# Performance work log

Measured on AMD Instinct MI355X. Metric: run time of the kernel, lower is better.

## Reference

```python
import jax, jax.numpy as jnp
import numpy as np

N = 50000      # nodes
E = 1600000    # edges
L = 128        # latent_size


def _mlp(h, W1, b1, W2, b2):
    # MLP(in_dim, [L, L]) == Linear -> ReLU -> Linear
    return jax.nn.relu(h @ W1 + b1) @ W2 + b2


def setup_inputs() -> dict:
    key = jax.random.key(0)
    ks = jax.random.split(key, 12)
    glorot = lambda k, i, o: jax.random.normal(k, (i, o), jnp.float32) * (2.0 / (i + o)) ** 0.5
    return {
        "pos": jax.random.normal(ks[0], (N, 3), jnp.float32),
        "x": jax.random.normal(ks[1], (N, L), jnp.float32),
        "edge_attr": jax.random.normal(ks[2], (E, L), jnp.float32),
        "edge_index": jax.random.randint(ks[3], (2, E), 0, N, jnp.int64),
        "last_pred": jax.random.normal(ks[4], (N, 3), jnp.float32),
        "mask_idx": jax.random.randint(ks[5], (N, 1), 0, 2, jnp.int32).astype(bool),
        # pos_embedding MLP params (in=3)
        "Wp1": glorot(ks[6], 3, L), "bp1": jnp.zeros((L,), jnp.float32),
        "Wp2": glorot(ks[7], L, L), "bp2": jnp.zeros((L,), jnp.float32),
        # dis_embedding MLP params (in=1)
        "Wd1": glorot(ks[8], 1, L), "bd1": jnp.zeros((L,), jnp.float32),
        "Wd2": glorot(ks[9], L, L), "bd2": jnp.zeros((L,), jnp.float32),
    }


def reference(pos, x, edge_attr, edge_index, last_pred, mask_idx,
              Wp1, bp1, Wp2, bp2, Wd1, bd1, Wd2, bd2):
    # mode == 'mask': replace masked node positions with last prediction
    pos = jnp.where(mask_idx, last_pred, pos)                    # [N,3]
    extended_x = x + _mlp(pos, Wp1, bp1, Wp2, bp2)               # [N,L]
    row, col = edge_index[0], edge_index[1]
    diff = pos[row] - pos[col]                                   # [E,3]
    length = jnp.linalg.norm(diff, axis=-1, keepdims=True)       # [E,1]
    extended_edge_attr = edge_attr + _mlp(length, Wd1, bd1, Wd2, bd2)  # [E,L]
    return extended_x, extended_edge_attr
```

## Files before the change

### kernel.cpp

```cpp
#include <hip/hip_runtime.h>
#include <hip/hip_bf16.h>

#define NN 50000
#define EE 1600000
#define NB_NODE 391
#define NIV 129

typedef float f32x4 __attribute__((ext_vector_type(4)));
typedef __bf16 bf16x8 __attribute__((ext_vector_type(8)));

__device__ float gT[128];
__device__ __align__(16) float gA[NIV * 128];
__device__ __align__(16) float gB[NIV * 128];

__device__ __forceinline__ float edge_len(int e, const int* __restrict__ eidx,
                                          const float* __restrict__ pos,
                                          const float* __restrict__ lp,
                                          const int* __restrict__ msk) {
    int ri = eidx[e];
    int ci = eidx[EE + e];
    const float* pr = msk[ri] ? lp : pos;
    const float* pc = msk[ci] ? lp : pos;
    float dx = pr[3 * ri + 0] - pc[3 * ci + 0];
    float dy = pr[3 * ri + 1] - pc[3 * ci + 1];
    float dz = pr[3 * ri + 2] - pc[3 * ci + 2];
    return sqrtf(dx * dx + dy * dy + dz * dz);
}

union SM {
    struct {
        __bf16 w2l[16384];
        float w1l[384], b1l[128], b2l[128];
        float tbuf[8][512];
    } n;
    struct {
        float t_s[128];
        int   rank_s[128];
        float pa[4][128], pb[4][128];
    } p;
};

__device__ __forceinline__ void stage_w2(const float* __restrict__ W2, __bf16* w2l) {
    for (int idx = threadIdx.x; idx < 128 * 128; idx += 512) {
        int k = idx >> 7;
        int c = idx & 127;
        int dst = (((k >> 5) * 8 + (c >> 4)) * 64 + (((k >> 3) & 3) * 16 + (c & 15))) * 8 + (k & 7);
        w2l[dst] = (__bf16)W2[idx];
    }
}

__global__ __launch_bounds__(512, 3) void node_prep_kernel(
    const float* __restrict__ pos, const float* __restrict__ x,
    const float* __restrict__ lp, const int* __restrict__ msk,
    const float* __restrict__ Wp1, const float* __restrict__ bp1,
    const float* __restrict__ Wp2, const float* __restrict__ bp2,
    const float* __restrict__ Wd1, const float* __restrict__ bd1,
    const float* __restrict__ Wd2, const float* __restrict__ bd2,
    float* __restrict__ outx)
{
    __shared__ SM sm;

    if (blockIdx.x >= NB_NODE) {
        const int i = blockIdx.x - NB_NODE;
        const int c = threadIdx.x & 127;
        const int q = threadIdx.x >> 7;
        if (q == 0) {
            float w1 = Wd1[c], b1 = bd1[c];
            sm.p.t_s[c] = (w1 == 0.f) ? __builtin_inff() : (-b1 / w1);
        }
        __syncthreads();
        if (q == 0) {
            float t = sm.p.t_s[c];
            int rank = 0;
            for (int j = 0; j < 128; j++) {
                float tj = sm.p.t_s[j];
                rank += (tj < t) || (tj == t && j < c);
            }
            sm.p.rank_s[c] = rank;
            if (i == 0) gT[rank] = t;
        }
        __syncthreads();
        float a = 0.f, b = 0.f;
        for (int kk = 0; kk < 32; kk++) {
            int k = q * 32 + kk;
            float w1k = Wd1[k], b1k = bd1[k];
            bool act = (w1k > 0.f) ? (sm.p.rank_s[k] < i)
                     : (w1k < 0.f) ? (sm.p.rank_s[k] >= i)
                                   : (b1k > 0.f);
            if (act) {
                float w2 = Wd2[k * 128 + c];
                a = fmaf(w1k, w2, a);
                b = fmaf(b1k, w2, b);
            }
        }
        sm.p.pa[q][c] = a;
        sm.p.pb[q][c] = b;
        __syncthreads();
        if (q == 0) {
            float A = sm.p.pa[0][c] + sm.p.pa[1][c] + sm.p.pa[2][c] + sm.p.pa[3][c];
            float B = sm.p.pb[0][c] + sm.p.pb[1][c] + sm.p.pb[2][c] + sm.p.pb[3][c];
            gA[i * 128 + c] = A;
            gB[i * 128 + c] = B + bd2[c];
        }
        return;
    }

    stage_w2(Wp2, sm.n.w2l);
    for (int i = threadIdx.x; i < 384; i += 512) sm.n.w1l[i] = Wp1[i];
    if (threadIdx.x < 128) {
        sm.n.b1l[threadIdx.x] = bp1[threadIdx.x];
        sm.n.b2l[threadIdx.x] = bp2[threadIdx.x];
    }
    __syncthreads();

    const int w = threadIdx.x >> 6;
    const int l = threadIdx.x & 63;
    const int llo = l & 15;
    const int lgrp = l >> 4;
    float* tb = sm.n.tbuf[w];

    const int e0 = blockIdx.x * 128 + w * 16;
    const bool valid = (e0 + 16 <= NN);

    f32x4 ear[8];
    f32x4 acc[8];
    if (valid) {
        const float* srow = x + (size_t)e0 * 128;
#pragma unroll
        for (int j = 0; j < 8; j++) ear[j] = *(const f32x4*)(srow + j * 256 + l * 4);

        int nd = e0 + llo;
        const float* p = msk[nd] ? lp : pos;
        float px = p[3 * nd + 0];
        float py = p[3 * nd + 1];
        float pz = p[3 * nd + 2];

#pragma unroll
        for (int m = 0; m < 8; m++) acc[m] = (f32x4){0.f, 0.f, 0.f, 0.f};

#pragma unroll
        for (int kk = 0; kk < 4; kk++) {
            bf16x8 hf;
#pragma unroll
            for (int j = 0; j < 8; j++) {
                int k = kk * 32 + lgrp * 8 + j;
                float h = px * sm.n.w1l[k] + py * sm.n.w1l[128 + k]
                        + pz * sm.n.w1l[256 + k] + sm.n.b1l[k];
                hf[j] = (__bf16)fmaxf(h, 0.f);
            }
#pragma unroll
            for (int m = 0; m < 8; m++) {
                bf16x8 wf = *(const bf16x8*)&sm.n.w2l[((kk * 8 + m) * 64 + l) * 8];
                acc[m] = __builtin_amdgcn_mfma_f32_16x16x32_bf16(wf, hf, acc[m], 0, 0, 0);
            }
        }
    }

    float* drow = outx + (size_t)e0 * 128;
    f32x4 b2v = *(const f32x4*)&sm.n.b2l[(l & 31) * 4];

#pragma unroll
    for (int p = 0; p < 4; p++) {
        if (valid && (llo >> 2) == p) {
            int r = llo & 3;
#pragma unroll
            for (int m = 0; m < 8; m++) {
                int c = (m * 16 + lgrp * 4 + r * 4) & 127;
                *(f32x4*)&tb[r * 128 + c] = acc[m];
            }
        }
        __syncthreads();
        if (valid) {
#pragma unroll
            for (int i = 0; i < 2; i++) {
                int row = 2 * i + (l >> 5);
                int c = ((l & 31) * 4 + row * 4) & 127;
                f32x4 tv = *(const f32x4*)&tb[row * 128 + c];
                f32x4 o = tv + b2v + ear[p * 2 + i];
                *(f32x4*)(drow + p * 512 + i * 256 + l * 4) = o;
            }
        }
        __syncthreads();
    }
}

__global__ __launch_bounds__(256) void edge_kernel(
    const float* __restrict__ ea, const int* __restrict__ eidx,
    const float* __restrict__ pos, const float* __restrict__ lp,
    const int* __restrict__ msk, float* __restrict__ oute)
{
    __shared__ float ts[128];
    if (threadIdx.x < 128) ts[threadIdx.x] = gT[threadIdx.x];
    __syncthreads();

    const int g  = threadIdx.x >> 5;
    const int c4 = (threadIdx.x & 31) * 4;

    for (int r0 = (blockIdx.x * 8 + g) * 4; r0 < EE; r0 += gridDim.x * 32) {
        f32x4 e[4];
#pragma unroll
        for (int j = 0; j < 4; j++)
            e[j] = *(const f32x4*)(ea + (size_t)(r0 + j) * 128 + c4);

        float lenv[4];
        int iv[4];
#pragma unroll
        for (int j = 0; j < 4; j++) {
            lenv[j] = edge_len(r0 + j, eidx, pos, lp, msk);
            int lo = 0;
#pragma unroll
            for (int s = 128; s > 0; s >>= 1) {
                int m = lo + s;
                if (m <= 128 && ts[m - 1] < lenv[j]) lo = m;
            }
            iv[j] = lo;
        }

#pragma unroll
        for (int j = 0; j < 4; j++) {
            const f32x4 a = *(const f32x4*)&gA[iv[j] * 128 + c4];
            const f32x4 b = *(const f32x4*)&gB[iv[j] * 128 + c4];
            *(f32x4*)(oute + (size_t)(r0 + j) * 128 + c4) = e[j] + (lenv[j] * a + b);
        }
    }
}

extern "C" void kernel_launch(void* const* d_in, const int* in_sizes, int n_in,
                              void* d_out, int out_size, void* d_ws, size_t ws_size,
                              hipStream_t stream) {
    const float* pos        = (const float*)d_in[0];
    const float* x          = (const float*)d_in[1];
    const float* edge_attr  = (const float*)d_in[2];
    const int* edge_index   = (const int*)d_in[3];
    const float* last_pred  = (const float*)d_in[4];
    const int* mask         = (const int*)d_in[5];
    const float* Wp1 = (const float*)d_in[6];
    const float* bp1 = (const float*)d_in[7];
    const float* Wp2 = (const float*)d_in[8];
    const float* bp2 = (const float*)d_in[9];
    const float* Wd1 = (const float*)d_in[10];
    const float* bd1 = (const float*)d_in[11];
    const float* Wd2 = (const float*)d_in[12];
    const float* bd2 = (const float*)d_in[13];

    float* outx = (float*)d_out;
    float* oute = outx + (size_t)NN * 128;

    node_prep_kernel<<<NB_NODE + NIV, 512, 0, stream>>>(
        pos, x, last_pred, mask,
        Wp1, bp1, Wp2, bp2, Wd1, bd1, Wd2, bd2, outx);

    edge_kernel<<<2048, 256, 0, stream>>>(
        edge_attr, edge_index, pos, last_pred, mask, oute);
}
```

Before: 379.9 us.

## Precompute edge lengths and bin indices in separate kernel before streaming pass

Adds a pre-pass kernel that computes each edge's length and piecewise-linear bin index once per edge and writes them as float2 to the workspace. The main edge kernel then reads these values instead of doing gathers and a binary search per lane. It also remaps lanes so one wavefront covers two full 128-float rows per load. This removes the redundant per-lane gather and search latency from the bandwidth-bound pass, at the cost of an extra launch and 12.8MB of additional traffic.

```diff
diff --git a/kernel.cpp b/kernel.cpp
--- a/kernel.cpp
+++ b/kernel.cpp
@@ -184,43 +184,78 @@
     }
 }
 
-__global__ __launch_bounds__(256) void edge_kernel(
-    const float* __restrict__ ea, const int* __restrict__ eidx,
-    const float* __restrict__ pos, const float* __restrict__ lp,
-    const int* __restrict__ msk, float* __restrict__ oute)
+__global__ __launch_bounds__(256) void leniv_kernel(
+    const int* __restrict__ eidx, const float* __restrict__ pos,
+    const float* __restrict__ lp, const int* __restrict__ msk,
+    float2* __restrict__ lenivp)
 {
     __shared__ float ts[128];
     if (threadIdx.x < 128) ts[threadIdx.x] = gT[threadIdx.x];
     __syncthreads();
-
-    const int g  = threadIdx.x >> 5;
-    const int c4 = (threadIdx.x & 31) * 4;
-
-    for (int r0 = (blockIdx.x * 8 + g) * 4; r0 < EE; r0 += gridDim.x * 32) {
+    int e = blockIdx.x * 256 + threadIdx.x;
+    if (e < EE) {
+        float lv = edge_len(e, eidx, pos, lp, msk);
+        int lo = 0;
+#pragma unroll
+        for (int s = 128; s > 0; s >>= 1) {
+            int m = lo + s;
+            if (m <= 128 && ts[m - 1] < lv) lo = m;
+        }
+        lenivp[e] = make_float2(lv, (float)lo);
+    }
+}
+
+template <bool PRE>
+__global__ __launch_bounds__(256) void edge_kernel(
+    const float* __restrict__ ea, const float2* __restrict__ lenivp,
+    const int* __restrict__ eidx, const float* __restrict__ pos,
+    const float* __restrict__ lp, const int* __restrict__ msk,
+    float* __restrict__ oute)
+{
+    __shared__ float ts[128];
+    if (!PRE) {
+        if (threadIdx.x < 128) ts[threadIdx.x] = gT[threadIdx.x];
+        __syncthreads();
+    }
+
+    const int w  = threadIdx.x >> 6;
+    const int l  = threadIdx.x & 63;
+    const int c4 = (l & 31) * 4;
+    const int rh = l >> 5;
+
+    for (int base = blockIdx.x * 32 + w * 8; base < EE; base += gridDim.x * 32) {
         f32x4 e[4];
 #pragma unroll
         for (int j = 0; j < 4; j++)
-            e[j] = *(const f32x4*)(ea + (size_t)(r0 + j) * 128 + c4);
+            e[j] = *(const f32x4*)(ea + (size_t)(base + 2 * j) * 128 + l * 4);
 
         float lenv[4];
         int iv[4];
 #pragma unroll
         for (int j = 0; j < 4; j++) {
-            lenv[j] = edge_len(r0 + j, eidx, pos, lp, msk);
-            int lo = 0;
-#pragma unroll
-            for (int s = 128; s > 0; s >>= 1) {
-                int m = lo + s;
-                if (m <= 128 && ts[m - 1] < lenv[j]) lo = m;
-            }
-            iv[j] = lo;
+            int r = base + 2 * j + rh;
+            if (PRE) {
+                float2 f2 = lenivp[r];
+                lenv[j] = f2.x;
+                iv[j] = (int)f2.y;
+            } else {
+                lenv[j] = edge_len(r, eidx, pos, lp, msk);
+                int lo = 0;
+#pragma unroll
+                for (int s = 128; s > 0; s >>= 1) {
+                    int m = lo + s;
+                    if (m <= 128 && ts[m - 1] < lenv[j]) lo = m;
+                }
+                iv[j] = lo;
+            }
         }
 
 #pragma unroll
         for (int j = 0; j < 4; j++) {
             const f32x4 a = *(const f32x4*)&gA[iv[j] * 128 + c4];
             const f32x4 b = *(const f32x4*)&gB[iv[j] * 128 + c4];
-            *(f32x4*)(oute + (size_t)(r0 + j) * 128 + c4) = e[j] + (lenv[j] * a + b);
+            *(f32x4*)(oute + (size_t)(base + 2 * j) * 128 + l * 4) =
+                e[j] + (lenv[j] * a + b);
         }
     }
 }
@@ -250,6 +285,14 @@
         pos, x, last_pred, mask,
         Wp1, bp1, Wp2, bp2, Wd1, bd1, Wd2, bd2, outx);
 
-    edge_kernel<<<2048, 256, 0, stream>>>(
-        edge_attr, edge_index, pos, last_pred, mask, oute);
-}
+    if (ws_size >= (size_t)EE * 8) {
+        float2* lenivp = (float2*)d_ws;
+        leniv_kernel<<<(EE + 255) / 256, 256, 0, stream>>>(
+            edge_index, pos, last_pred, mask, lenivp);
+        edge_kernel<true><<<2048, 256, 0, stream>>>(
+            edge_attr, lenivp, edge_index, pos, last_pred, mask, oute);
+    } else {
+        edge_kernel<false><<<2048, 256, 0, stream>>>(
+            edge_attr, nullptr, edge_index, pos, last_pred, mask, oute);
+    }
+}
```

Result: faster. 368.1 us, median of 2 (-3.1%).

## Split table prep into tiny kernel and fuse node and edge work into one kernel

Applied to the files above, without the earlier changes.

The piecewise-linear lookup tables for the distance MLP now come from a small separate kernel. Node-MLP blocks and edge blocks run together in one mega kernel, so node work overlaps the memory-bound edge stream instead of running as its own launch. Edge blocks now use 512 threads and load the next stride's edge_attr rows early, which is meant to hide memory latency. The cost is an extra tiny serial launch and 512-thread edge blocks that share occupancy limits (launch bounds 512,3 and the large node shared memory) with the node blocks.

```diff
diff --git a/kernel.cpp b/kernel.cpp
--- a/kernel.cpp
+++ b/kernel.cpp
@@ -4,6 +4,7 @@
 #define NN 50000
 #define EE 1600000
 #define NB_NODE 391
+#define NB_EDGE 2048
 #define NIV 129
 
 typedef float f32x4 __attribute__((ext_vector_type(4)));
@@ -27,6 +28,41 @@
     return sqrtf(dx * dx + dy * dy + dz * dz);
 }
 
+__global__ void prep_tables(const float* __restrict__ Wd1, const float* __restrict__ bd1,
+                            const float* __restrict__ Wd2, const float* __restrict__ bd2) {
+    __shared__ float t_s[128];
+    __shared__ int rank_s[128];
+    const int c = threadIdx.x;
+    float w1 = Wd1[c], b1 = bd1[c];
+    float t = (w1 == 0.f) ? __builtin_inff() : (-b1 / w1);
+    t_s[c] = t;
+    __syncthreads();
+    int rank = 0;
+    for (int j = 0; j < 128; j++) {
+        float tj = t_s[j];
+        rank += (tj < t) || (tj == t && j < c);
+    }
+    rank_s[c] = rank;
+    if (blockIdx.x == 0) gT[rank] = t;
+    __syncthreads();
+
+    const int i = blockIdx.x;
+    float a = 0.f, b = 0.f;
+    for (int k = 0; k < 128; k++) {
+        float w1k = Wd1[k], b1k = bd1[k];
+        bool act = (w1k > 0.f) ? (rank_s[k] < i)
+                 : (w1k < 0.f) ? (rank_s[k] >= i)
+                               : (b1k > 0.f);
+        if (act) {
+            float w2 = Wd2[k * 128 + c];
+            a = fmaf(w1k, w2, a);
+            b = fmaf(b1k, w2, b);
+        }
+    }
+    gA[i * 128 + c] = a;
+    gB[i * 128 + c] = b + bd2[c];
+}
+
 union SM {
     struct {
         __bf16 w2l[16384];
@@ -34,10 +70,8 @@
         float tbuf[8][512];
     } n;
     struct {
-        float t_s[128];
-        int   rank_s[128];
-        float pa[4][128], pb[4][128];
-    } p;
+        float ts[128];
+    } e;
 };
 
 __device__ __forceinline__ void stage_w2(const float* __restrict__ W2, __bf16* w2l) {
@@ -49,58 +83,72 @@
     }
 }
 
-__global__ __launch_bounds__(512, 3) void node_prep_kernel(
+__global__ __launch_bounds__(512, 3) void mega_kernel(
     const float* __restrict__ pos, const float* __restrict__ x,
+    const float* __restrict__ ea, const int* __restrict__ eidx,
     const float* __restrict__ lp, const int* __restrict__ msk,
     const float* __restrict__ Wp1, const float* __restrict__ bp1,
     const float* __restrict__ Wp2, const float* __restrict__ bp2,
-    const float* __restrict__ Wd1, const float* __restrict__ bd1,
-    const float* __restrict__ Wd2, const float* __restrict__ bd2,
-    float* __restrict__ outx)
+    float* __restrict__ outx, float* __restrict__ oute)
 {
     __shared__ SM sm;
 
+    const int w = threadIdx.x >> 6;
+    const int l = threadIdx.x & 63;
+
     if (blockIdx.x >= NB_NODE) {
-        const int i = blockIdx.x - NB_NODE;
-        const int c = threadIdx.x & 127;
-        const int q = threadIdx.x >> 7;
-        if (q == 0) {
-            float w1 = Wd1[c], b1 = bd1[c];
-            sm.p.t_s[c] = (w1 == 0.f) ? __builtin_inff() : (-b1 / w1);
-        }
+        if (threadIdx.x < 128) sm.e.ts[threadIdx.x] = gT[threadIdx.x];
         __syncthreads();
-        if (q == 0) {
-            float t = sm.p.t_s[c];
-            int rank = 0;
-            for (int j = 0; j < 128; j++) {
-                float tj = sm.p.t_s[j];
-                rank += (tj < t) || (tj == t && j < c);
-            }
-            sm.p.rank_s[c] = rank;
-            if (i == 0) gT[rank] = t;
-        }
-        __syncthreads();
-        float a = 0.f, b = 0.f;
-        for (int kk = 0; kk < 32; kk++) {
-            int k = q * 32 + kk;
-            float w1k = Wd1[k], b1k = bd1[k];
-            bool act = (w1k > 0.f) ? (sm.p.rank_s[k] < i)
-                     : (w1k < 0.f) ? (sm.p.rank_s[k] >= i)
-                                   : (b1k > 0.f);
-            if (act) {
-                float w2 = Wd2[k * 128 + c];
-                a = fmaf(w1k, w2, a);
-                b = fmaf(b1k, w2, b);
-            }
-        }
-        sm.p.pa[q][c] = a;
-        sm.p.pb[q][c] = b;
-        __syncthreads();
-        if (q == 0) {
-            float A = sm.p.pa[0][c] + sm.p.pa[1][c] + sm.p.pa[2][c] + sm.p.pa[3][c];
-            float B = sm.p.pb[0][c] + sm.p.pb[1][c] + sm.p.pb[2][c] + sm.p.pb[3][c];
-            gA[i * 128 + c] = A;
-            gB[i * 128 + c] = B + bd2[c];
+
+        const int rh = l >> 5;
+        const int c4 = (l & 31) * 4;
+        const int stride = NB_EDGE * 64;
+
+        int base = (blockIdx.x - NB_NODE) * 64 + w * 8;
+        if (base >= EE) return;
+
+        f32x4 e[4];
+#pragma unroll
+        for (int j = 0; j < 4; j++)
+            e[j] = *(const f32x4*)(ea + (size_t)(base + 2 * j) * 128 + l * 4);
+
+        while (true) {
+            const int nbase = base + stride;
+
+            float lenv[4];
+            int iv[4];
+#pragma unroll
+            for (int j = 0; j < 4; j++) {
+                int r = base + 2 * j + rh;
+                lenv[j] = edge_len(r, eidx, pos, lp, msk);
+                int lo = 0;
+#pragma unroll
+                for (int s = 128; s > 0; s >>= 1) {
+                    int m = lo + s;
+                    if (m <= 128 && sm.e.ts[m - 1] < lenv[j]) lo = m;
+                }
+                iv[j] = lo;
+            }
+
+            f32x4 en[4];
+            if (nbase < EE) {
+#pragma unroll
+                for (int j = 0; j < 4; j++)
+                    en[j] = *(const f32x4*)(ea + (size_t)(nbase + 2 * j) * 128 + l * 4);
+            }
+
+#pragma unroll
+            for (int j = 0; j < 4; j++) {
+                const f32x4 a = *(const f32x4*)&gA[iv[j] * 128 + c4];
+                const f32x4 b = *(const f32x4*)&gB[iv[j] * 128 + c4];
+                *(f32x4*)(oute + (size_t)(base + 2 * j) * 128 + l * 4) =
+                    e[j] + (lenv[j] * a + b);
+            }
+
+            if (nbase >= EE) break;
+            base = nbase;
+#pragma unroll
+            for (int j = 0; j < 4; j++) e[j] = en[j];
         }
         return;
     }
@@ -113,8 +161,6 @@
     }
     __syncthreads();
 
-    const int w = threadIdx.x >> 6;
-    const int l = threadIdx.x & 63;
     const int llo = l & 15;
     const int lgrp = l >> 4;
     float* tb = sm.n.tbuf[w];
@@ -181,47 +227,6 @@
             }
         }
         __syncthreads();
-    }
-}
-
-__global__ __launch_bounds__(256) void edge_kernel(
-    const float* __restrict__ ea, const int* __restrict__ eidx,
-    const float* __restrict__ pos, const float* __restrict__ lp,
-    const int* __restrict__ msk, float* __restrict__ oute)
-{
-    __shared__ float ts[128];
-    if (threadIdx.x < 128) ts[threadIdx.x] = gT[threadIdx.x];
-    __syncthreads();
-
-    const int g  = threadIdx.x >> 5;
-    const int c4 = (threadIdx.x & 31) * 4;
-
-    for (int r0 = (blockIdx.x * 8 + g) * 4; r0 < EE; r0 += gridDim.x * 32) {
-        f32x4 e[4];
-#pragma unroll
-        for (int j = 0; j < 4; j++)
-            e[j] = *(const f32x4*)(ea + (size_t)(r0 + j) * 128 + c4);
-
-        float lenv[4];
-        int iv[4];
-#pragma unroll
-        for (int j = 0; j < 4; j++) {
-            lenv[j] = edge_len(r0 + j, eidx, pos, lp, msk);
-            int lo = 0;
-#pragma unroll
-            for (int s = 128; s > 0; s >>= 1) {
-                int m = lo + s;
-                if (m <= 128 && ts[m - 1] < lenv[j]) lo = m;
-            }
-            iv[j] = lo;
-        }
-
-#pragma unroll
-        for (int j = 0; j < 4; j++) {
-            const f32x4 a = *(const f32x4*)&gA[iv[j] * 128 + c4];
-            const f32x4 b = *(const f32x4*)&gB[iv[j] * 128 + c4];
-            *(f32x4*)(oute + (size_t)(r0 + j) * 128 + c4) = e[j] + (lenv[j] * a + b);
-        }
     }
 }
 
@@ -246,10 +251,9 @@
     float* outx = (float*)d_out;
     float* oute = outx + (size_t)NN * 128;
 
-    node_prep_kernel<<<NB_NODE + NIV, 512, 0, stream>>>(
-        pos, x, last_pred, mask,
-        Wp1, bp1, Wp2, bp2, Wd1, bd1, Wd2, bd2, outx);
-
-    edge_kernel<<<2048, 256, 0, stream>>>(
-        edge_attr, edge_index, pos, last_pred, mask, oute);
-}
+    prep_tables<<<NIV, 128, 0, stream>>>(Wd1, bd1, Wd2, bd2);
+
+    mega_kernel<<<NB_NODE + NB_EDGE, 512, 0, stream>>>(
+        pos, x, edge_attr, edge_index, last_pred, mask,
+        Wp1, bp1, Wp2, bp2, outx, oute);
+}
```

New measurement: 491.6 us. 29.4% more time.
